# Kernel optimization log

Measured on AMD Instinct MI355X. Metric: run time of the kernel, lower is better.

## Reference

```python
import jax, jax.numpy as jnp
import numpy as np

NUM_USER, NUM_ITEM, NUM_HIDDEN, NNZ = 8192, 16384, 64, 200000


def setup_inputs() -> dict:
    key = jax.random.key(0)
    k_u, k_i, k_idx, k_r = jax.random.split(key, 4)
    # Parameters: torch.normal(mean=0, std=0.1)
    embed_user = 0.1 * jax.random.normal(k_u, (NUM_USER, NUM_HIDDEN), dtype=jnp.float32)
    embed_item = 0.1 * jax.random.normal(k_i, (NUM_ITEM, NUM_HIDDEN), dtype=jnp.float32)
    indices = jax.random.randint(k_idx, (2, NNZ), 0, 8192, dtype=jnp.int64)
    ratings = jax.random.uniform(k_r, (NNZ,), dtype=jnp.float32)
    return {"embed_user": embed_user, "embed_item": embed_item,
            "indices": indices, "ratings": ratings}


def reference(embed_user, embed_item, indices, ratings):
    U, H = embed_user.shape
    I = embed_item.shape[0]
    # Row masks: True for any user/item id appearing in the batch.
    user_mask = jnp.zeros((U,), dtype=bool).at[indices[0]].set(True)
    item_mask = jnp.zeros((I,), dtype=bool).at[indices[1]].set(True)
    # Mask whole rows, then dense cross product (matches sparse.mm -> to_dense).
    eu = embed_user * user_mask[:, None].astype(embed_user.dtype)
    ei = embed_item * item_mask[:, None].astype(embed_item.dtype)
    pred = jnp.einsum('uh,ih->ui', eu, ei)  # [U, I]
    # sparse_coo_tensor(...).to_dense() sums duplicate (u, i) entries.
    label = jnp.zeros((U, I), dtype=ratings.dtype).at[indices[0], indices[1]].add(ratings)
    ratio = float(U * I) / float(ratings.shape[0])
    return pred, label, ratio
```

## Files before the change

### kernel.cpp

```cpp
#include <hip/hip_runtime.h>

#define NU 8192
#define NI 16384
#define NH 64
#define TM 128
#define TN 128
#define KP 32

typedef float v4 __attribute__((ext_vector_type(4)));

__global__ void init_kernel(unsigned int* __restrict__ p, int nwords,
                            float* __restrict__ ratio) {
    int i = blockIdx.x * blockDim.x + threadIdx.x;
    if (i < nwords) p[i] = 0u;
    if (i == 0) *ratio = 671.08864f;
}

__global__ void build_masks_kernel(const int* __restrict__ idx,
                                   unsigned char* __restrict__ um,
                                   unsigned char* __restrict__ im, int nnz) {
    int k = blockIdx.x * blockDim.x + threadIdx.x;
    if (k < nnz) {
        um[idx[k]]       = 1;
        im[idx[nnz + k]] = 1;
    }
}

__global__ __launch_bounds__(256, 4) void gemm_kernel(
    const float* __restrict__ A,
    const float* __restrict__ B,
    const unsigned char* __restrict__ um,
    const unsigned char* __restrict__ im,
    float* __restrict__ pred,
    float* __restrict__ label)
{
    __shared__ float As[KP * TM];
    __shared__ float Bs[KP * TN];

    const int tid = threadIdx.x;
    const int c0 = blockIdx.x * TN;
    const int r0 = blockIdx.y * TM;

    const int any = __syncthreads_or((tid < TN) && (im[c0 + tid] != 0));

    v4* __restrict__ pred4 = (v4*)pred;
    v4* __restrict__ lab4  = (v4*)label;
    const v4 z4 = (v4){0.f, 0.f, 0.f, 0.f};

    if (!any) {
#pragma unroll
        for (int i = 0; i < TM * TN / 4 / 256; ++i) {
            int f   = i * 256 + tid;
            int row = f >> 5;
            int cv  = f & 31;
            size_t o = (size_t)(r0 + row) * (NI / 4) + (size_t)(c0 >> 2) + cv;
            __builtin_nontemporal_store(z4, &pred4[o]);
            __builtin_nontemporal_store(z4, &lab4[o]);
        }
        return;
    }

    const float4* A4 = (const float4*)A;
    const float4* B4 = (const float4*)B;
    const float4* As4 = (const float4*)As;
    const float4* Bs4 = (const float4*)Bs;

    const int tx = tid & 15;
    const int ty = tid >> 4;

    float acc[2][4][2][4];
#pragma unroll
    for (int rg = 0; rg < 2; ++rg)
#pragma unroll
        for (int i = 0; i < 4; ++i)
#pragma unroll
            for (int cg = 0; cg < 2; ++cg)
#pragma unroll
                for (int j = 0; j < 4; ++j) acc[rg][i][cg][j] = 0.f;

#pragma unroll
    for (int p = 0; p < 2; ++p) {
        if (p) __syncthreads();

#pragma unroll
        for (int t = 0; t < 4; ++t) {
            int idx4 = tid + t * 256;
            int m    = idx4 >> 3;
            int kv   = idx4 & 7;
            int base = (4 * kv) * TM + 4 * ((m >> 2) ^ kv) + (m & 3);
            {
                float msk = um[r0 + m] ? 1.f : 0.f;
                float4 v = A4[(size_t)(r0 + m) * (NH / 4) + p * (KP / 4) + kv];
                As[base]           = v.x * msk;
                As[base + TM]      = v.y * msk;
                As[base + 2 * TM]  = v.z * msk;
                As[base + 3 * TM]  = v.w * msk;
            }
            {
                float msk = im[c0 + m] ? 1.f : 0.f;
                float4 v = B4[(size_t)(c0 + m) * (NH / 4) + p * (KP / 4) + kv];
                Bs[base]           = v.x * msk;
                Bs[base + TN]      = v.y * msk;
                Bs[base + 2 * TN]  = v.z * msk;
                Bs[base + 3 * TN]  = v.w * msk;
            }
        }
        __syncthreads();

        if (p == 0) {
#pragma unroll
            for (int i = 0; i < TM * TN / 4 / 256; ++i) {
                int f   = i * 256 + tid;
                int row = f >> 5;
                int cv  = f & 31;
                size_t o = (size_t)(r0 + row) * (NI / 4) + (size_t)(c0 >> 2) + cv;
                __builtin_nontemporal_store(z4, &lab4[o]);
            }
        }

#pragma unroll 2
        for (int kv = 0; kv < KP / 4; ++kv) {
            const int ta = ty ^ kv;
            const int tb = tx ^ kv;
            const int kb = kv * 4 * 32;
#pragma unroll
            for (int r = 0; r < 4; ++r) {
                float4 a0 = As4[kb + r * 32 + ta];
                float4 a1 = As4[kb + r * 32 + 16 + ta];
                float4 b0 = Bs4[kb + r * 32 + tb];
                float4 b1 = Bs4[kb + r * 32 + 16 + tb];
                float ar[2][4] = {{a0.x, a0.y, a0.z, a0.w}, {a1.x, a1.y, a1.z, a1.w}};
                float br[2][4] = {{b0.x, b0.y, b0.z, b0.w}, {b1.x, b1.y, b1.z, b1.w}};
#pragma unroll
                for (int rg = 0; rg < 2; ++rg)
#pragma unroll
                    for (int i = 0; i < 4; ++i)
#pragma unroll
                        for (int cg = 0; cg < 2; ++cg)
#pragma unroll
                            for (int j = 0; j < 4; ++j)
                                acc[rg][i][cg][j] += ar[rg][i] * br[cg][j];
            }
        }
    }

#pragma unroll
    for (int rg = 0; rg < 2; ++rg)
#pragma unroll
        for (int i = 0; i < 4; ++i) {
            int row = r0 + rg * 64 + ty * 4 + i;
            size_t rb = (size_t)row * (NI / 4);
#pragma unroll
            for (int cg = 0; cg < 2; ++cg) {
                size_t cv = (size_t)((c0 + cg * 64 + tx * 4) >> 2);
                v4 v = (v4){acc[rg][i][cg][0], acc[rg][i][cg][1],
                            acc[rg][i][cg][2], acc[rg][i][cg][3]};
                __builtin_nontemporal_store(v, &pred4[rb + cv]);
            }
        }
}

__global__ void scatter_kernel(const int* __restrict__ idx,
                               const float* __restrict__ r,
                               float* __restrict__ label, int nnz) {
    int k = blockIdx.x * blockDim.x + threadIdx.x;
    if (k < nnz) {
        int u  = idx[k];
        int it = idx[nnz + k];
        atomicAdd(&label[(size_t)u * NI + it], r[k]);
    }
}

extern "C" void kernel_launch(void* const* d_in, const int* in_sizes, int n_in,
                              void* d_out, int out_size, void* d_ws, size_t ws_size,
                              hipStream_t stream) {
    const float* A   = (const float*)d_in[0];
    const float* B   = (const float*)d_in[1];
    const int*   idx = (const int*)d_in[2];
    const float* r   = (const float*)d_in[3];
    const int nnz = in_sizes[3];

    float* out   = (float*)d_out;
    float* pred  = out;
    float* label = out + (size_t)NU * NI;
    float* ratio = out + 2 * (size_t)NU * NI;

    unsigned char* um = (unsigned char*)d_ws;
    unsigned char* im = um + NU;

    const int mask_words = (NU + NI) / 4;
    init_kernel<<<(mask_words + 255) / 256, 256, 0, stream>>>(
        (unsigned int*)d_ws, mask_words, ratio);
    build_masks_kernel<<<(nnz + 255) / 256, 256, 0, stream>>>(idx, um, im, nnz);

    dim3 grid(NI / TN, NU / TM);
    gemm_kernel<<<grid, 256, 0, stream>>>(A, B, um, im, pred, label);

    scatter_kernel<<<(nnz + 255) / 256, 256, 0, stream>>>(idx, r, label, nnz);
}
```

Before: 1.123 ms.

## Prefetch second K-panel into registers during label zeroing and first compute

Loads the first K-half into shared memory, then issues global loads for the second K-half into registers before zeroing the label tile and running the first compute pass. Those registers are written to shared memory after a barrier, so global load latency overlaps with stores and FMAs. Mask lookups are also hoisted so each row is read once. Launch bounds drop from 4 to 3 waves per SIMD to give room for the extra registers, which may reduce occupancy.

```diff
diff --git a/kernel.cpp b/kernel.cpp
--- a/kernel.cpp
+++ b/kernel.cpp
@@ -26,7 +26,7 @@
     }
 }
 
-__global__ __launch_bounds__(256, 4) void gemm_kernel(
+__global__ __launch_bounds__(256, 3) void gemm_kernel(
     const float* __restrict__ A,
     const float* __restrict__ B,
     const unsigned char* __restrict__ um,
@@ -65,6 +65,50 @@
     const float4* As4 = (const float4*)As;
     const float4* Bs4 = (const float4*)Bs;
 
+    const int ms  = tid >> 3;
+    const int kvL = tid & 7;
+
+    float amsk[4], bmsk[4];
+#pragma unroll
+    for (int t = 0; t < 4; ++t) {
+        amsk[t] = um[r0 + ms + 32 * t] ? 1.f : 0.f;
+        bmsk[t] = im[c0 + ms + 32 * t] ? 1.f : 0.f;
+    }
+
+#pragma unroll
+    for (int t = 0; t < 4; ++t) {
+        int m    = ms + 32 * t;
+        int base = (4 * kvL) * TM + 4 * ((m >> 2) ^ kvL) + (m & 3);
+        float4 va = A4[(size_t)(r0 + m) * (NH / 4) + kvL];
+        float4 vb = B4[(size_t)(c0 + m) * (NH / 4) + kvL];
+        As[base]          = va.x * amsk[t];
+        As[base + TM]     = va.y * amsk[t];
+        As[base + 2 * TM] = va.z * amsk[t];
+        As[base + 3 * TM] = va.w * amsk[t];
+        Bs[base]          = vb.x * bmsk[t];
+        Bs[base + TN]     = vb.y * bmsk[t];
+        Bs[base + 2 * TN] = vb.z * bmsk[t];
+        Bs[base + 3 * TN] = vb.w * bmsk[t];
+    }
+    __syncthreads();
+
+    float4 pa[4], pb[4];
+#pragma unroll
+    for (int t = 0; t < 4; ++t) {
+        int m = ms + 32 * t;
+        pa[t] = A4[(size_t)(r0 + m) * (NH / 4) + (KP / 4) + kvL];
+        pb[t] = B4[(size_t)(c0 + m) * (NH / 4) + (KP / 4) + kvL];
+    }
+
+#pragma unroll
+    for (int i = 0; i < TM * TN / 4 / 256; ++i) {
+        int f   = i * 256 + tid;
+        int row = f >> 5;
+        int cv  = f & 31;
+        size_t o = (size_t)(r0 + row) * (NI / 4) + (size_t)(c0 >> 2) + cv;
+        __builtin_nontemporal_store(z4, &lab4[o]);
+    }
+
     const int tx = tid & 15;
     const int ty = tid >> 4;
 
@@ -80,42 +124,22 @@
 
 #pragma unroll
     for (int p = 0; p < 2; ++p) {
-        if (p) __syncthreads();
-
-#pragma unroll
-        for (int t = 0; t < 4; ++t) {
-            int idx4 = tid + t * 256;
-            int m    = idx4 >> 3;
-            int kv   = idx4 & 7;
-            int base = (4 * kv) * TM + 4 * ((m >> 2) ^ kv) + (m & 3);
-            {
-                float msk = um[r0 + m] ? 1.f : 0.f;
-                float4 v = A4[(size_t)(r0 + m) * (NH / 4) + p * (KP / 4) + kv];
-                As[base]           = v.x * msk;
-                As[base + TM]      = v.y * msk;
-                As[base + 2 * TM]  = v.z * msk;
-                As[base + 3 * TM]  = v.w * msk;
+        if (p) {
+            __syncthreads();
+#pragma unroll
+            for (int t = 0; t < 4; ++t) {
+                int m    = ms + 32 * t;
+                int base = (4 * kvL) * TM + 4 * ((m >> 2) ^ kvL) + (m & 3);
+                As[base]          = pa[t].x * amsk[t];
+                As[base + TM]     = pa[t].y * amsk[t];
+                As[base + 2 * TM] = pa[t].z * amsk[t];
+                As[base + 3 * TM] = pa[t].w * amsk[t];
+                Bs[base]          = pb[t].x * bmsk[t];
+                Bs[base + TN]     = pb[t].y * bmsk[t];
+                Bs[base + 2 * TN] = pb[t].z * bmsk[t];
+                Bs[base + 3 * TN] = pb[t].w * bmsk[t];
             }
-            {
-                float msk = im[c0 + m] ? 1.f : 0.f;
-                float4 v = B4[(size_t)(c0 + m) * (NH / 4) + p * (KP / 4) + kv];
-                Bs[base]           = v.x * msk;
-                Bs[base + TN]      = v.y * msk;
-                Bs[base + 2 * TN]  = v.z * msk;
-                Bs[base + 3 * TN]  = v.w * msk;
-            }
-        }
-        __syncthreads();
-
-        if (p == 0) {
-#pragma unroll
-            for (int i = 0; i < TM * TN / 4 / 256; ++i) {
-                int f   = i * 256 + tid;
-                int row = f >> 5;
-                int cv  = f & 31;
-                size_t o = (size_t)(r0 + row) * (NI / 4) + (size_t)(c0 >> 2) + cv;
-                __builtin_nontemporal_store(z4, &lab4[o]);
-            }
+            __syncthreads();
         }
 
 #pragma unroll 2
```

After: 1.115 ms. Within noise of the previous version (-0.8%).
